# Optimization experiments

Measured on AMD Instinct MI355X. Metric: run time of the kernel, lower is better.

## Reference

```python
import jax, jax.numpy as jnp
import numpy as np

N = 100000      # nodes
E = 1200000     # edges
K = 512         # TopKPooling ratio=512 -> fixed k
EPS = 1e-7      # GENConv message eps
BN_EPS = 1e-5   # BatchNorm eps
NEG_SLOPE = 0.01  # LeakyReLU default


def _lin_init(key, fan_in, fan_out):
    k1, k2 = jax.random.split(key)
    s = 1.0 / np.sqrt(fan_in)
    w = jax.random.uniform(k1, (fan_in, fan_out), minval=-s, maxval=s, dtype=jnp.float32)
    b = jax.random.uniform(k2, (fan_out,), minval=-s, maxval=s, dtype=jnp.float32)
    return w, b


def setup_inputs() -> dict:
    key = jax.random.key(0)
    ks = jax.random.split(key, 12)
    pos = jax.random.normal(ks[0], (N, 3), dtype=jnp.float32)
    edge_index = jax.random.randint(ks[1], (2, E), 0, N, dtype=jnp.int64)
    # GENConv(3, 16): lin_src + MLP [16, 32, 16] (BatchNorm+ReLU on hidden)
    c1_lw, c1_lb = _lin_init(ks[2], 3, 16)
    c1_w1, c1_b1 = _lin_init(ks[3], 16, 32)
    c1_g1 = jnp.ones((32,), jnp.float32); c1_be1 = jnp.zeros((32,), jnp.float32)
    c1_w2, c1_b2 = _lin_init(ks[4], 32, 16)
    # GENConv(16, 64): lin_src + MLP [64, 128, 64]
    c2_lw, c2_lb = _lin_init(ks[5], 16, 64)
    c2_w1, c2_b1 = _lin_init(ks[6], 64, 128)
    c2_g1 = jnp.ones((128,), jnp.float32); c2_be1 = jnp.zeros((128,), jnp.float32)
    c2_w2, c2_b2 = _lin_init(ks[7], 128, 64)
    # TopKPooling score weight [in_channels]
    pool_w = jax.random.uniform(ks[8], (64,), minval=-1.0/8, maxval=1.0/8, dtype=jnp.float32)
    return dict(pos=pos, edge_index=edge_index,
                c1_lw=c1_lw, c1_lb=c1_lb, c1_w1=c1_w1, c1_b1=c1_b1,
                c1_g1=c1_g1, c1_be1=c1_be1, c1_w2=c1_w2, c1_b2=c1_b2,
                c2_lw=c2_lw, c2_lb=c2_lb, c2_w1=c2_w1, c2_b1=c2_b1,
                c2_g1=c2_g1, c2_be1=c2_be1, c2_w2=c2_w2, c2_b2=c2_b2,
                pool_w=pool_w)


def _genconv(x, src, dst, lw, lb, w1, b1, g1, be1, w2, b2):
    # lin_src (in_channels != out_channels)
    x = x @ lw + lb                                   # [N, C]
    # message: relu(x_j) + eps
    msg = jax.nn.relu(x[src]) + EPS                   # [E, C]
    # softmax aggregation (t = 1.0), per destination, per channel
    m = jax.ops.segment_max(msg, dst, num_segments=N) # [N, C]
    a = jnp.exp(msg - m[dst])
    denom = jax.ops.segment_sum(a, dst, num_segments=N)
    alpha = a / (denom[dst] + 1e-16)
    out = jax.ops.segment_sum(msg * alpha, dst, num_segments=N)
    out = out + x                                     # residual with dst features
    # MLP: Linear -> BatchNorm (train-mode stats) -> ReLU -> Linear
    h = out @ w1 + b1
    mu = h.mean(axis=0)
    var = h.var(axis=0)
    h = (h - mu) / jnp.sqrt(var + BN_EPS) * g1 + be1
    h = jax.nn.relu(h)
    return h @ w2 + b2


def reference(pos, edge_index,
              c1_lw, c1_lb, c1_w1, c1_b1, c1_g1, c1_be1, c1_w2, c1_b2,
              c2_lw, c2_lb, c2_w1, c2_b1, c2_g1, c2_be1, c2_w2, c2_b2,
              pool_w):
    src, dst = edge_index[0], edge_index[1]
    x = _genconv(pos, src, dst, c1_lw, c1_lb, c1_w1, c1_b1, c1_g1, c1_be1, c1_w2, c1_b2)
    x = jnp.where(x > 0, x, NEG_SLOPE * x)            # LeakyReLU
    x = _genconv(x, src, dst, c2_lw, c2_lb, c2_w1, c2_b1, c2_g1, c2_be1, c2_w2, c2_b2)
    x = jnp.where(x > 0, x, NEG_SLOPE * x)
    # TopKPooling: score = tanh(x . w / ||w||), select top K, gate selected features
    score = jnp.tanh((x @ pool_w) / jnp.linalg.norm(pool_w))  # [N]
    top_vals, perm = jax.lax.top_k(score, K)
    return x[perm] * top_vals[:, None]                # [K, 64]
```

## Files before the change

### kernel.cpp

```cpp
#include <hip/hip_runtime.h>
#include <stdint.h>

#define BLK 256

static constexpr float F_EPS = 1e-7f;
static constexpr float F_NEG = 0.01f;
static constexpr int   TOPK  = 512;
static constexpr int   NPART = 8;
static constexpr int   PBLK  = 128;

typedef unsigned long long u64;

__device__ __forceinline__ unsigned int ord_f32(float f) {
  unsigned int u = __float_as_uint(f);
  return (u & 0x80000000u) ? ~u : (u | 0x80000000u);
}

template<int CIN, int COUT, int TM, bool BN, bool LEAKY, bool STAT>
__global__ __launch_bounds__(256) void gemm_tile(const float* __restrict__ in,
    const float* __restrict__ W, const float* __restrict__ b,
    const float* __restrict__ scale, const float* __restrict__ shift,
    float* __restrict__ out, double* __restrict__ partial, int n) {
  constexpr int TN = COUT / 16;
  constexpr int NODES = 16 * TM;
  constexpr int KC = (CIN > 64) ? 64 : CIN;
  constexpr int NPAD = NODES + 4;
  __shared__ float xs[KC][NPAD];
  __shared__ float wsh[CIN * COUT];
  __shared__ float sB[COUT];
  __shared__ float sSc[BN ? CIN : 4];
  __shared__ float sSh[BN ? CIN : 4];
  for (int i = threadIdx.x; i < CIN * COUT; i += 256) wsh[i] = W[i];
  for (int i = threadIdx.x; i < COUT; i += 256) sB[i] = b[i];
  if constexpr (BN) {
    for (int i = threadIdx.x; i < CIN; i += 256) { sSc[i] = scale[i]; sSh[i] = shift[i]; }
  }
  __syncthreads();
  const int tn = threadIdx.x & 15;
  const int tj = threadIdx.x >> 4;
  const int node0 = blockIdx.x * NODES;

  float acc[TM][TN];
  #pragma unroll
  for (int m = 0; m < TM; ++m)
    #pragma unroll
    for (int j = 0; j < TN; ++j) acc[m][j] = sB[tj * TN + j];

  for (int kc = 0; kc < CIN; kc += KC) {
    __syncthreads();
    constexpr int NL = NODES * (KC / 4);
    for (int i = threadIdx.x; i < NL; i += 256) {
      int nd = i / (KC / 4);
      int kq = i - nd * (KC / 4);
      int gn = node0 + nd;
      const float* p = in + (size_t)(gn < n ? gn : n - 1) * CIN + kc + kq * 4;
      float4 v = *reinterpret_cast<const float4*>(p);
      if constexpr (BN) {
        int kb = kc + kq * 4;
        v.x = fmaxf(v.x * sSc[kb+0] + sSh[kb+0], 0.f);
        v.y = fmaxf(v.y * sSc[kb+1] + sSh[kb+1], 0.f);
        v.z = fmaxf(v.z * sSc[kb+2] + sSh[kb+2], 0.f);
        v.w = fmaxf(v.w * sSc[kb+3] + sSh[kb+3], 0.f);
      }
      xs[kq*4+0][nd] = v.x; xs[kq*4+1][nd] = v.y;
      xs[kq*4+2][nd] = v.z; xs[kq*4+3][nd] = v.w;
    }
    __syncthreads();
    #pragma unroll 16
    for (int k = 0; k < KC; ++k) {
      float xv[TM], wv[TN];
      #pragma unroll
      for (int m = 0; m < TM; ++m) xv[m] = xs[k][tn * TM + m];
      #pragma unroll
      for (int j = 0; j < TN; ++j) wv[j] = wsh[(kc + k) * COUT + tj * TN + j];
      #pragma unroll
      for (int m = 0; m < TM; ++m)
        #pragma unroll
        for (int j = 0; j < TN; ++j)
          acc[m][j] += xv[m] * wv[j];
    }
  }
  #pragma unroll
  for (int m = 0; m < TM; ++m) {
    int gn = node0 + tn * TM + m;
    if (gn < n) {
      float* orow = out + (size_t)gn * COUT + tj * TN;
      #pragma unroll
      for (int j = 0; j < TN; j += 4) {
        float a0 = acc[m][j], a1 = acc[m][j+1], a2 = acc[m][j+2], a3 = acc[m][j+3];
        if constexpr (LEAKY) {
          a0 = a0 > 0.f ? a0 : F_NEG * a0;
          a1 = a1 > 0.f ? a1 : F_NEG * a1;
          a2 = a2 > 0.f ? a2 : F_NEG * a2;
          a3 = a3 > 0.f ? a3 : F_NEG * a3;
        }
        float4 r; r.x = a0; r.y = a1; r.z = a2; r.w = a3;
        *reinterpret_cast<float4*>(orow + j) = r;
      }
    }
  }
  if constexpr (STAT) {
    __shared__ double sStat[2 * COUT];
    double sv[TN], qv[TN];
    #pragma unroll
    for (int j = 0; j < TN; ++j) { sv[j] = 0.0; qv[j] = 0.0; }
    #pragma unroll
    for (int m = 0; m < TM; ++m) {
      bool v = (node0 + tn * TM + m) < n;
      #pragma unroll
      for (int j = 0; j < TN; ++j) {
        double a = v ? (double)acc[m][j] : 0.0;
        sv[j] += a; qv[j] += a * a;
      }
    }
    #pragma unroll
    for (int j = 0; j < TN; ++j) {
      for (int off = 8; off; off >>= 1) {
        sv[j] += __shfl_down(sv[j], off, 16);
        qv[j] += __shfl_down(qv[j], off, 16);
      }
    }
    if (tn == 0) {
      #pragma unroll
      for (int j = 0; j < TN; ++j) {
        sStat[tj * TN + j] = sv[j];
        sStat[COUT + tj * TN + j] = qv[j];
      }
    }
    __syncthreads();
    for (int i = threadIdx.x; i < 2 * COUT; i += 256)
      partial[(size_t)blockIdx.x * (2 * COUT) + i] = sStat[i];
  }
}

template<int COUT>
__global__ __launch_bounds__(256) void bn_fin_ws(const double* __restrict__ partial,
    const float* __restrict__ g, const float* __restrict__ be,
    float* __restrict__ sc, float* __restrict__ sh, int n, int nbx) {
  int j = blockIdx.x;
  int t = threadIdx.x;
  double s = 0, q = 0;
  for (int bdx = t; bdx < nbx; bdx += 256) {
    s += partial[(size_t)bdx * (2 * COUT) + j];
    q += partial[(size_t)bdx * (2 * COUT) + COUT + j];
  }
  for (int off = 32; off; off >>= 1) { s += __shfl_down(s, off); q += __shfl_down(q, off); }
  __shared__ double sw[4][2];
  int lane = t & 63, wid = t >> 6;
  if (lane == 0) { sw[wid][0] = s; sw[wid][1] = q; }
  __syncthreads();
  if (t == 0) {
    s = sw[0][0] + sw[1][0] + sw[2][0] + sw[3][0];
    q = sw[0][1] + sw[1][1] + sw[2][1] + sw[3][1];
    double inv_n = 1.0 / (double)n;
    double mu = s * inv_n;
    double var = q * inv_n - mu * mu;
    double scd = (double)g[j] / sqrt(var + 1e-5);
    sc[j] = (float)scd;
    sh[j] = (float)((double)be[j] - mu * scd);
  }
}

template<int CIN, int COUT, int JT, bool STAT = false>
__global__ __launch_bounds__(BLK) void lin_kernel(const float* __restrict__ in,
    const float* __restrict__ W, const float* __restrict__ b,
    float* __restrict__ out, double* __restrict__ partial, int n) {
  __shared__ float sW[CIN * JT];
  __shared__ float sB[JT];
  const int j0 = blockIdx.y * JT;
  for (int i = threadIdx.x; i < CIN * JT; i += BLK) {
    int k = i / JT, jj = i - k * JT;
    sW[i] = W[k * COUT + j0 + jj];
  }
  for (int i = threadIdx.x; i < JT; i += BLK) sB[i] = b[j0 + i];
  __syncthreads();
  int node = blockIdx.x * BLK + threadIdx.x;
  bool valid = node < n;
  if constexpr (!STAT) { if (!valid) return; }
  int rnode = valid ? node : (n - 1);
  float acc[JT];
  #pragma unroll
  for (int jj = 0; jj < JT; ++jj) acc[jj] = sB[jj];
  const float* xrow = in + (size_t)rnode * CIN;
  if constexpr ((CIN & 3) == 0) {
    float x[CIN];
    #pragma unroll
    for (int k4 = 0; k4 < CIN / 4; ++k4) {
      float4 v = *reinterpret_cast<const float4*>(xrow + k4 * 4);
      x[4*k4+0] = v.x; x[4*k4+1] = v.y; x[4*k4+2] = v.z; x[4*k4+3] = v.w;
    }
    #pragma unroll
    for (int k = 0; k < CIN; ++k) {
      #pragma unroll
      for (int jj = 0; jj < JT; ++jj)
        acc[jj] += x[k] * sW[k * JT + jj];
    }
  } else {
    #pragma unroll
    for (int k = 0; k < CIN; ++k) {
      float xv = xrow[k];
      #pragma unroll
      for (int jj = 0; jj < JT; ++jj)
        acc[jj] += xv * sW[k * JT + jj];
    }
  }
  if (valid) {
    float* orow = out + (size_t)node * COUT + j0;
    #pragma unroll
    for (int jj = 0; jj < JT; jj += 4) {
      float4 r; r.x = acc[jj]; r.y = acc[jj+1]; r.z = acc[jj+2]; r.w = acc[jj+3];
      *reinterpret_cast<float4*>(orow + jj) = r;
    }
  }
  if constexpr (STAT) {
    __shared__ double sStat[4][2 * JT];
    int lane = threadIdx.x & 63, wid = threadIdx.x >> 6;
    #pragma unroll
    for (int jj = 0; jj < JT; ++jj) {
      double sv = valid ? (double)acc[jj] : 0.0;
      double qv = sv * sv;
      for (int off = 32; off; off >>= 1) {
        sv += __shfl_down(sv, off);
        qv += __shfl_down(qv, off);
      }
      if (lane == 0) { sStat[wid][jj] = sv; sStat[wid][JT + jj] = qv; }
    }
    __syncthreads();
    if (threadIdx.x < 2 * JT) {
      double v = sStat[0][threadIdx.x] + sStat[1][threadIdx.x]
               + sStat[2][threadIdx.x] + sStat[3][threadIdx.x];
      partial[((size_t)blockIdx.y * gridDim.x + blockIdx.x) * (2 * JT) + threadIdx.x] = v;
    }
  }
}

template<int COUT, int JT>
__global__ __launch_bounds__(256) void bn_fin3(const double* __restrict__ partial,
    const float* __restrict__ g, const float* __restrict__ be,
    float* __restrict__ sc, float* __restrict__ sh, int n, int nbx) {
  int j = blockIdx.x;
  int t = threadIdx.x;
  int jt = j / JT, jj = j - jt * JT;
  double s = 0, q = 0;
  for (int b = t; b < nbx; b += 256) {
    const double* row = partial + ((size_t)jt * nbx + b) * (2 * JT);
    s += row[jj];
    q += row[JT + jj];
  }
  for (int off = 32; off; off >>= 1) { s += __shfl_down(s, off); q += __shfl_down(q, off); }
  __shared__ double sw[4][2];
  int lane = t & 63, wid = t >> 6;
  if (lane == 0) { sw[wid][0] = s; sw[wid][1] = q; }
  __syncthreads();
  if (t == 0) {
    s = sw[0][0] + sw[1][0] + sw[2][0] + sw[3][0];
    q = sw[0][1] + sw[1][1] + sw[2][1] + sw[3][1];
    double inv_n = 1.0 / (double)n;
    double mu = s * inv_n;
    double var = q * inv_n - mu * mu;
    double scd = (double)g[j] / sqrt(var + 1e-5);
    sc[j] = (float)scd;
    sh[j] = (float)((double)be[j] - mu * scd);
  }
}

template<int CIN, int COUT, int JT>
__global__ __launch_bounds__(BLK) void mlp2_kernel(const float* __restrict__ h,
    const float* __restrict__ scale, const float* __restrict__ shift,
    const float* __restrict__ W, const float* __restrict__ b,
    float* __restrict__ out, int n) {
  __shared__ float sW[CIN * JT];
  __shared__ float sB[JT];
  __shared__ float sSc[CIN];
  __shared__ float sSh[CIN];
  const int j0 = blockIdx.y * JT;
  for (int i = threadIdx.x; i < CIN * JT; i += BLK) {
    int k = i / JT, jj = i - k * JT;
    sW[i] = W[k * COUT + j0 + jj];
  }
  for (int i = threadIdx.x; i < JT; i += BLK) sB[i] = b[j0 + i];
  for (int i = threadIdx.x; i < CIN; i += BLK) { sSc[i] = scale[i]; sSh[i] = shift[i]; }
  __syncthreads();
  int node = blockIdx.x * BLK + threadIdx.x;
  if (node >= n) return;
  float acc[JT];
  #pragma unroll
  for (int jj = 0; jj < JT; ++jj) acc[jj] = sB[jj];
  const float* xrow = h + (size_t)node * CIN;
  float x[CIN];
  #pragma unroll
  for (int k4 = 0; k4 < CIN / 4; ++k4) {
    float4 v = *reinterpret_cast<const float4*>(xrow + k4 * 4);
    x[4*k4+0] = fmaxf(v.x * sSc[4*k4+0] + sSh[4*k4+0], 0.f);
    x[4*k4+1] = fmaxf(v.y * sSc[4*k4+1] + sSh[4*k4+1], 0.f);
    x[4*k4+2] = fmaxf(v.z * sSc[4*k4+2] + sSh[4*k4+2], 0.f);
    x[4*k4+3] = fmaxf(v.w * sSc[4*k4+3] + sSh[4*k4+3], 0.f);
  }
  #pragma unroll
  for (int k = 0; k < CIN; ++k) {
    #pragma unroll
    for (int jj = 0; jj < JT; ++jj)
      acc[jj] += x[k] * sW[k * JT + jj];
  }
  float* orow = out + (size_t)node * COUT + j0;
  #pragma unroll
  for (int jj = 0; jj < JT; jj += 4) {
    float a0 = acc[jj], a1 = acc[jj+1], a2 = acc[jj+2], a3 = acc[jj+3];
    a0 = a0 > 0.f ? a0 : F_NEG * a0;
    a1 = a1 > 0.f ? a1 : F_NEG * a1;
    a2 = a2 > 0.f ? a2 : F_NEG * a2;
    a3 = a3 > 0.f ? a3 : F_NEG * a3;
    float4 r; r.x = a0; r.y = a1; r.z = a2; r.w = a3;
    *reinterpret_cast<float4*>(orow + jj) = r;
  }
}

__global__ __launch_bounds__(BLK) void deg_kernel(const int* __restrict__ dst,
    int* __restrict__ deg, int E) {
  int e = blockIdx.x * BLK + threadIdx.x;
  if (e < E) atomicAdd(&deg[dst[e]], 1);
}

__global__ __launch_bounds__(BLK) void blocksum_kernel(const int* __restrict__ deg,
    int* __restrict__ bsum, int n) {
  int i = blockIdx.x * BLK + threadIdx.x;
  int v = (i < n) ? deg[i] : 0;
  for (int off = 32; off; off >>= 1) v += __shfl_down(v, off);
  __shared__ int wsum[4];
  int lane = threadIdx.x & 63, wid = threadIdx.x >> 6;
  if (lane == 0) wsum[wid] = v;
  __syncthreads();
  if (threadIdx.x == 0) bsum[blockIdx.x] = wsum[0] + wsum[1] + wsum[2] + wsum[3];
}

__global__ __launch_bounds__(512) void scanb_kernel(int* __restrict__ bsum, int nb) {
  __shared__ int s[512];
  int t = threadIdx.x;
  int orig = (t < nb) ? bsum[t] : 0;
  s[t] = orig;
  __syncthreads();
  for (int off = 1; off < 512; off <<= 1) {
    int add = (t >= off) ? s[t - off] : 0;
    __syncthreads();
    s[t] += add;
    __syncthreads();
  }
  if (t < nb) bsum[t] = s[t] - orig;
}

__global__ __launch_bounds__(BLK) void rowstart_kernel(const int* __restrict__ deg,
    const int* __restrict__ bsum, int* __restrict__ rowstart,
    int* __restrict__ cursor, int n) {
  __shared__ int s[BLK];
  int t = threadIdx.x, i = blockIdx.x * BLK + t;
  int orig = (i < n) ? deg[i] : 0;
  s[t] = orig;
  __syncthreads();
  for (int off = 1; off < BLK; off <<= 1) {
    int add = (t >= off) ? s[t - off] : 0;
    __syncthreads();
    s[t] += add;
    __syncthreads();
  }
  if (i < n) { int st = bsum[blockIdx.x] + s[t] - orig; rowstart[i] = st; cursor[i] = st; }
}

__global__ __launch_bounds__(BLK) void scatter_kernel(const int* __restrict__ src,
    const int* __restrict__ dst, int* __restrict__ cursor, int* __restrict__ eidx,
    int E, int n) {
  const int r = blockIdx.x & (NPART - 1);
  const int sb = blockIdx.x >> 3;
  const int nsb = gridDim.x >> 3;
  for (int e = sb * BLK + threadIdx.x; e < E; e += nsb * BLK) {
    int d = dst[e];
    int dr = (int)(((unsigned long long)(unsigned)d * NPART) / (unsigned)n);
    if (dr == r) {
      int p = atomicAdd(&cursor[d], 1);
      eidx[p] = src[e];
    }
  }
}

template<int C>
__global__ __launch_bounds__(BLK) void agg_kernel(const int* __restrict__ rowstart,
    const int* __restrict__ deg, const int* __restrict__ eidx,
    const float* __restrict__ x, float* __restrict__ out, int n) {
  int gid = blockIdx.x * BLK + threadIdx.x;
  int node, c;
  if constexpr (C == 64) {
    node = __builtin_amdgcn_readfirstlane(gid >> 6);
    c = threadIdx.x & 63;
  } else {
    node = gid / C;
    c = gid & (C - 1);
  }
  if (node >= n) return;
  int s0, d;
  if constexpr (C == 64) {
    s0 = __builtin_amdgcn_readfirstlane(rowstart[node]);
    d  = __builtin_amdgcn_readfirstlane(deg[node]);
  } else {
    s0 = rowstart[node];
    d  = deg[node];
  }
  const float* xc = x + c;
  const int* ep = eidx + s0;
  float den = 0.f, num = 0.f;
  int nq = d >> 2;
  int i0 = 0, i1 = 0, i2 = 0, i3 = 0;
  int j0 = 0, j1 = 0, j2 = 0, j3 = 0;
  if (nq > 0) { i0 = ep[0]; i1 = ep[1]; i2 = ep[2]; i3 = ep[3]; }
  if (nq > 1) { j0 = ep[4]; j1 = ep[5]; j2 = ep[6]; j3 = ep[7]; }
  int q = 0;
  for (; q + 1 < nq; q += 2) {
    float xa = xc[(unsigned)i0 * C];
    float xb = xc[(unsigned)i1 * C];
    float xcv = xc[(unsigned)i2 * C];
    float xd = xc[(unsigned)i3 * C];
    float ya = xc[(unsigned)j0 * C];
    float yb = xc[(unsigned)j1 * C];
    float yc = xc[(unsigned)j2 * C];
    float yd = xc[(unsigned)j3 * C];
    if (q + 2 < nq) {
      const int* p2 = ep + (q + 2) * 4;
      i0 = p2[0]; i1 = p2[1]; i2 = p2[2]; i3 = p2[3];
    }
    if (q + 3 < nq) {
      const int* p3 = ep + (q + 3) * 4;
      j0 = p3[0]; j1 = p3[1]; j2 = p3[2]; j3 = p3[3];
    }
    float ma = fmaxf(xa, 0.f) + F_EPS;
    float mb = fmaxf(xb, 0.f) + F_EPS;
    float mc = fmaxf(xcv, 0.f) + F_EPS;
    float md = fmaxf(xd, 0.f) + F_EPS;
    float na = fmaxf(ya, 0.f) + F_EPS;
    float nb = fmaxf(yb, 0.f) + F_EPS;
    float nc = fmaxf(yc, 0.f) + F_EPS;
    float nd = fmaxf(yd, 0.f) + F_EPS;
    float aa = __expf(ma), ab = __expf(mb), ac = __expf(mc), ad = __expf(md);
    float ba = __expf(na), bb = __expf(nb), bc = __expf(nc), bd = __expf(nd);
    den += ((aa + ab) + (ac + ad)) + ((ba + bb) + (bc + bd));
    num += ((ma * aa + mb * ab) + (mc * ac + md * ad))
         + ((na * ba + nb * bb) + (nc * bc + nd * bd));
  }
  if (q < nq) {
    float xa = xc[(unsigned)i0 * C];
    float xb = xc[(unsigned)i1 * C];
    float xcv = xc[(unsigned)i2 * C];
    float xd = xc[(unsigned)i3 * C];
    float ma = fmaxf(xa, 0.f) + F_EPS;
    float mb = fmaxf(xb, 0.f) + F_EPS;
    float mc = fmaxf(xcv, 0.f) + F_EPS;
    float md = fmaxf(xd, 0.f) + F_EPS;
    float aa = __expf(ma), ab = __expf(mb), ac = __expf(mc), ad = __expf(md);
    den += (aa + ab) + (ac + ad);
    num += (ma * aa + mb * ab) + (mc * ac + md * ad);
  }
  for (int j = nq * 4; j < d; ++j) {
    int sA = ep[j];
    float xa = xc[(unsigned)sA * C];
    float ma = fmaxf(xa, 0.f) + F_EPS;
    float aa = __expf(ma);
    den += aa;
    num += ma * aa;
  }
  float xdv = xc[(unsigned)node * C];
  out[(size_t)node * C + c] = num / (den + 1e-16f) + xdv;
}

__global__ __launch_bounds__(BLK) void score_kernel(const float* __restrict__ x,
    const float* __restrict__ w, float* __restrict__ scores,
    u64* __restrict__ keys, int* __restrict__ ghist, int n) {
  __shared__ float sw[64];
  __shared__ float snorm;
  __shared__ int hl[256];
  if (threadIdx.x < 64) sw[threadIdx.x] = w[threadIdx.x];
  hl[threadIdx.x] = 0;
  __syncthreads();
  if (threadIdx.x < 64) {
    float v = sw[threadIdx.x];
    float sq = v * v;
    for (int off = 32; off; off >>= 1) sq += __shfl_down(sq, off);
    if (threadIdx.x == 0) snorm = 1.f / sqrtf(sq);
  }
  __syncthreads();
  int node = blockIdx.x * BLK + threadIdx.x;
  if (node < n) {
    const float4* row = reinterpret_cast<const float4*>(x + (size_t)node * 64);
    float acc = 0.f;
    #pragma unroll
    for (int k4 = 0; k4 < 16; ++k4) {
      float4 v = row[k4];
      const float4 wv = *reinterpret_cast<const float4*>(&sw[4 * k4]);
      acc += v.x * wv.x + v.y * wv.y + v.z * wv.z + v.w * wv.w;
    }
    float s = tanhf(acc * snorm);
    scores[node] = s;
    u64 key = ((u64)ord_f32(s) << 17) | (u64)(0x1FFFF - node);
    keys[node] = key;
    atomicAdd(&hl[(int)(key >> 41)], 1);
  }
  __syncthreads();
  int v = hl[threadIdx.x];
  if (v) atomicAdd(&ghist[threadIdx.x], v);
}

__global__ void pick0_kernel(int* __restrict__ istate, const int* __restrict__ hist) {
  if (threadIdx.x == 0) {
    int k = TOPK, run = 0;
    for (int d = 255; d >= 0; --d) {
      int c = hist[d];
      if (run + c >= k) { istate[1] = d; istate[0] = k - run; break; }
      run += c;
    }
    istate[2] = 0; istate[4] = 0;
  }
}

__global__ __launch_bounds__(BLK) void compact0_kernel(const u64* __restrict__ in,
    u64* __restrict__ outb, u64* __restrict__ sel, int* __restrict__ istate, int n) {
  int i = blockIdx.x * BLK + threadIdx.x;
  if (i >= n) return;
  u64 kkey = in[i];
  int b = (int)(kkey >> 41);
  int digit = istate[1];
  if (b > digit) {
    sel[atomicAdd(&istate[2], 1)] = kkey;
  } else if (b == digit) {
    outb[atomicAdd(&istate[4], 1)] = kkey;
  }
}

__global__ __launch_bounds__(1024) void topk_finish(u64* __restrict__ bufB,
    u64* __restrict__ bufA, u64* __restrict__ sel, const int* __restrict__ istate,
    const float* __restrict__ scores, int* __restrict__ perm,
    float* __restrict__ gval) {
  __shared__ int hl[512];
  __shared__ int tsum[512];
  __shared__ u64 sk[512];
  __shared__ int sh_digit, sh_k, sh_sel, sh_out, sh_cnt;
  int t = threadIdx.x;
  if (t == 0) { sh_cnt = istate[4]; sh_k = istate[0]; sh_sel = istate[2]; }
  __syncthreads();
  u64* cur = bufB;
  u64* nxt = bufA;
  const int shifts[5] = {33, 25, 17, 9, 0};
  const int masks[5]  = {255, 255, 255, 255, 511};
  for (int r = 0; r < 5; ++r) {
    const int shift = shifts[r], mask = masks[r], wlen = mask + 1;
    for (int i = t; i < wlen; i += 1024) hl[i] = 0;
    __syncthreads();
    int cnt = sh_cnt, krem = sh_k;
    for (int i = t; i < cnt; i += 1024)
      atomicAdd(&hl[(int)(cur[i] >> shift) & mask], 1);
    __syncthreads();
    int v = 0;
    if (t < wlen) { v = hl[t]; tsum[t] = v; }
    __syncthreads();
    for (int off = 1; off < wlen; off <<= 1) {
      int add = 0;
      if (t + off < wlen) add = tsum[t + off];
      __syncthreads();
      if (t + off < wlen) tsum[t] += add;
      __syncthreads();
    }
    if (t < wlen) {
      int T = tsum[t];
      if (T >= krem && (T - v) < krem) {
        sh_digit = t;
        sh_k = krem - (T - v);
      }
    }
    if (t == 0) sh_out = 0;
    __syncthreads();
    int digit = sh_digit;
    for (int i = t; i < cnt; i += 1024) {
      u64 kk = cur[i];
      int b = (int)(kk >> shift) & mask;
      if (b > digit) sel[atomicAdd(&sh_sel, 1)] = kk;
      else if (b == digit) nxt[atomicAdd(&sh_out, 1)] = kk;
    }
    __syncthreads();
    if (t == 0) sh_cnt = sh_out;
    __syncthreads();
    u64* tmp = cur; cur = nxt; nxt = tmp;
  }
  int base = sh_sel, krem = sh_k;
  for (int i = t; i < krem; i += 1024) sel[base + i] = cur[i];
  __syncthreads();
  if (t < 512) sk[t] = sel[t];
  __syncthreads();
  if (t < 512) {
    u64 key = sk[t];
    int rank = 0;
    for (int j = 0; j < 512; ++j) rank += (sk[j] > key) ? 1 : 0;
    int node = 0x1FFFF - (int)(key & 0x1FFFFull);
    perm[rank] = node;
    gval[rank] = scores[node];
  }
}

__global__ __launch_bounds__(256) void gather_kernel(const int* __restrict__ perm,
    const float* __restrict__ gval, const float* __restrict__ x,
    float* __restrict__ out) {
  int i = blockIdx.x * 256 + threadIdx.x;
  int r = i >> 4, c = i & 15;
  int node = perm[r];
  float v = gval[r];
  float4 xv = reinterpret_cast<const float4*>(x)[(size_t)node * 16 + c];
  float4 o; o.x = xv.x * v; o.y = xv.y * v; o.z = xv.z * v; o.w = xv.w * v;
  reinterpret_cast<float4*>(out)[(size_t)r * 16 + c] = o;
}

extern "C" void kernel_launch(void* const* d_in, const int* in_sizes, int n_in,
                              void* d_out, int out_size, void* d_ws, size_t ws_size,
                              hipStream_t stream) {
  const int N = in_sizes[0] / 3;
  const int E = in_sizes[1] / 2;

  const float* pos   = (const float*)d_in[0];
  const int*   ei    = (const int*)d_in[1];
  const int*   src   = ei;
  const int*   dst   = ei + E;
  const float* c1_lw = (const float*)d_in[2];
  const float* c1_lb = (const float*)d_in[3];
  const float* c1_w1 = (const float*)d_in[4];
  const float* c1_b1 = (const float*)d_in[5];
  const float* c1_g1 = (const float*)d_in[6];
  const float* c1_be1= (const float*)d_in[7];
  const float* c1_w2 = (const float*)d_in[8];
  const float* c1_b2 = (const float*)d_in[9];
  const float* c2_lw = (const float*)d_in[10];
  const float* c2_lb = (const float*)d_in[11];
  const float* c2_w1 = (const float*)d_in[12];
  const float* c2_b1 = (const float*)d_in[13];
  const float* c2_g1 = (const float*)d_in[14];
  const float* c2_be1= (const float*)d_in[15];
  const float* c2_w2 = (const float*)d_in[16];
  const float* c2_b2 = (const float*)d_in[17];
  const float* poolw = (const float*)d_in[18];

  float* ws = (float*)d_ws;
  float* x1   = ws;
  float* h1   = ws + (size_t)16 * N;
  float* o1   = ws + (size_t)48 * N;
  float* res2 = ws;
  float* x2   = ws + (size_t)64 * N;
  float* res1 = x2;
  float* h2   = ws + (size_t)128 * N;
  float* o2   = ws + (size_t)256 * N;
  float* scores = ws + (size_t)320 * N;
  u64* candA = (u64*)(ws + (size_t)321 * N);
  u64* candB = candA + N;
  u64* sel   = candB + N;
  double* partial = (double*)(sel + TOPK);
  int* ibase   = (int*)(partial + (size_t)524288);
  int* istate  = ibase;
  int* hist    = ibase + 8;
  int* bsum    = ibase + 264;
  int* perm    = ibase + 776;
  float* gval  = (float*)(ibase + 1288);
  int* deg     = ibase + 1800;
  int* rowstart= deg + N;
  int* cursor  = rowstart + N;
  int* eidx    = cursor + N;
  float* fsc   = (float*)(eidx + E);
  float* sc1 = fsc;        float* sh1 = fsc + 32;
  float* sc2 = fsc + 64;   float* sh2 = fsc + 192;

  const int nbN = (N + BLK - 1) / BLK;
  const int nbE = (E + BLK - 1) / BLK;
  const int nbG = (N + 63) / 64;

  hipMemsetAsync(ibase, 0, (size_t)(1800 + N) * sizeof(int), stream);

  deg_kernel<<<nbE, BLK, 0, stream>>>(dst, deg, E);
  blocksum_kernel<<<nbN, BLK, 0, stream>>>(deg, bsum, N);
  scanb_kernel<<<1, 512, 0, stream>>>(bsum, nbN);
  rowstart_kernel<<<nbN, BLK, 0, stream>>>(deg, bsum, rowstart, cursor, N);
  scatter_kernel<<<NPART * PBLK, BLK, 0, stream>>>(src, dst, cursor, eidx, E, N);

  lin_kernel<3, 16, 16><<<dim3(nbN, 1), BLK, 0, stream>>>(pos, c1_lw, c1_lb, x1, nullptr, N);
  agg_kernel<16><<<(N * 16 + BLK - 1) / BLK, BLK, 0, stream>>>(rowstart, deg, eidx, x1, res1, N);
  lin_kernel<16, 32, 32, true><<<dim3(nbN, 1), BLK, 0, stream>>>(res1, c1_w1, c1_b1, h1, partial, N);
  bn_fin3<32, 32><<<32, 256, 0, stream>>>(partial, c1_g1, c1_be1, sc1, sh1, N, nbN);
  mlp2_kernel<32, 16, 16><<<dim3(nbN, 1), BLK, 0, stream>>>(h1, sc1, sh1, c1_w2, c1_b2, o1, N);

  gemm_tile<16, 64, 4, false, false, false><<<nbG, 256, 0, stream>>>(
      o1, c2_lw, c2_lb, nullptr, nullptr, x2, nullptr, N);
  agg_kernel<64><<<(N * 64 + BLK - 1) / BLK, BLK, 0, stream>>>(rowstart, deg, eidx, x2, res2, N);
  gemm_tile<64, 128, 4, false, false, true><<<nbG, 256, 0, stream>>>(
      res2, c2_w1, c2_b1, nullptr, nullptr, h2, partial, N);
  bn_fin_ws<128><<<128, 256, 0, stream>>>(partial, c2_g1, c2_be1, sc2, sh2, N, nbG);
  gemm_tile<128, 64, 4, true, true, false><<<nbG, 256, 0, stream>>>(
      h2, c2_w2, c2_b2, sc2, sh2, o2, nullptr, N);

  score_kernel<<<nbN, BLK, 0, stream>>>(o2, poolw, scores, candA, hist, N);
  pick0_kernel<<<1, 64, 0, stream>>>(istate, hist);
  compact0_kernel<<<nbN, BLK, 0, stream>>>(candA, candB, sel, istate, N);
  topk_finish<<<1, 1024, 0, stream>>>(candB, candA, sel, istate, scores, perm, gval);
  gather_kernel<<<32, 256, 0, stream>>>(perm, gval, o2, (float*)d_out);

  (void)n_in; (void)out_size; (void)ws_size;
}
```

Before: 381.0 us.

## Pre-bucket edges by destination partition before CSR scatter

```diff
diff --git a/kernel.cpp b/kernel.cpp
--- a/kernel.cpp
+++ b/kernel.cpp
@@ -8,6 +8,7 @@
 static constexpr int   TOPK  = 512;
 static constexpr int   NPART = 8;
 static constexpr int   PBLK  = 128;
+static constexpr int   PBN   = 1024;
 
 typedef unsigned long long u64;
 
@@ -365,19 +366,76 @@
   if (i < n) { int st = bsum[blockIdx.x] + s[t] - orig; rowstart[i] = st; cursor[i] = st; }
 }
 
-__global__ __launch_bounds__(BLK) void scatter_kernel(const int* __restrict__ src,
-    const int* __restrict__ dst, int* __restrict__ cursor, int* __restrict__ eidx,
-    int E, int n) {
+__global__ __launch_bounds__(BLK) void pcount_kernel(const int* __restrict__ dst,
+    int* __restrict__ pcnt, int E, int step, int chunk) {
+  __shared__ int c8[NPART];
+  if (threadIdx.x < NPART) c8[threadIdx.x] = 0;
+  __syncthreads();
+  int e0 = blockIdx.x * chunk;
+  int e1 = min(e0 + chunk, E);
+  for (int e = e0 + threadIdx.x; e < e1; e += BLK) {
+    int p = dst[e] / step;
+    if (p > NPART - 1) p = NPART - 1;
+    atomicAdd(&c8[p], 1);
+  }
+  __syncthreads();
+  if (threadIdx.x < NPART) pcnt[blockIdx.x * NPART + threadIdx.x] = c8[threadIdx.x];
+}
+
+__global__ __launch_bounds__(1024) void pscan_kernel(const int* __restrict__ pcnt,
+    int* __restrict__ poff, int* __restrict__ ptot, int nb) {
+  __shared__ int s[1024];
+  __shared__ int colbase;
+  int t = threadIdx.x;
+  if (t == 0) colbase = 0;
+  __syncthreads();
+  for (int p = 0; p < NPART; ++p) {
+    int orig = (t < nb) ? pcnt[t * NPART + p] : 0;
+    s[t] = orig;
+    __syncthreads();
+    for (int off = 1; off < 1024; off <<= 1) {
+      int add = (t >= off) ? s[t - off] : 0;
+      __syncthreads();
+      s[t] += add;
+      __syncthreads();
+    }
+    if (t < nb) poff[t * NPART + p] = colbase + s[t] - orig;
+    if (t == 0) ptot[p] = colbase;
+    __syncthreads();
+    if (t == 0) colbase += s[1023];
+    __syncthreads();
+  }
+  if (t == 0) ptot[NPART] = colbase;
+}
+
+__global__ __launch_bounds__(BLK) void ppack_kernel(const int* __restrict__ src,
+    const int* __restrict__ dst, const int* __restrict__ poff,
+    int2* __restrict__ pairbuf, int E, int step, int chunk) {
+  __shared__ int c8[NPART];
+  if (threadIdx.x < NPART) c8[threadIdx.x] = poff[blockIdx.x * NPART + threadIdx.x];
+  __syncthreads();
+  int e0 = blockIdx.x * chunk;
+  int e1 = min(e0 + chunk, E);
+  for (int e = e0 + threadIdx.x; e < e1; e += BLK) {
+    int d = dst[e], s = src[e];
+    int p = d / step;
+    if (p > NPART - 1) p = NPART - 1;
+    int pos = atomicAdd(&c8[p], 1);
+    pairbuf[pos] = make_int2(s, d);
+  }
+}
+
+__global__ __launch_bounds__(BLK) void scatter2_kernel(const int2* __restrict__ pairbuf,
+    const int* __restrict__ ptot, int* __restrict__ cursor, int* __restrict__ eidx) {
   const int r = blockIdx.x & (NPART - 1);
+  const int s0 = ptot[r];
+  const int s1 = ptot[r + 1];
   const int sb = blockIdx.x >> 3;
   const int nsb = gridDim.x >> 3;
-  for (int e = sb * BLK + threadIdx.x; e < E; e += nsb * BLK) {
-    int d = dst[e];
-    int dr = (int)(((unsigned long long)(unsigned)d * NPART) / (unsigned)n);
-    if (dr == r) {
-      int p = atomicAdd(&cursor[d], 1);
-      eidx[p] = src[e];
-    }
+  for (int i = s0 + sb * BLK + threadIdx.x; i < s1; i += nsb * BLK) {
+    int2 pr = pairbuf[i];
+    int p = atomicAdd(&cursor[pr.y], 1);
+    eidx[p] = pr.x;
   }
 }
 
@@ -667,10 +725,16 @@
   float* fsc   = (float*)(eidx + E);
   float* sc1 = fsc;        float* sh1 = fsc + 32;
   float* sc2 = fsc + 64;   float* sh2 = fsc + 192;
+  int2* pairbuf = (int2*)(((uintptr_t)(fsc + 320) + 7) & ~(uintptr_t)7);
+  int* pcnt = (int*)(pairbuf + E);
+  int* poff = pcnt + PBN * NPART;
+  int* ptot = poff + PBN * NPART;
 
   const int nbN = (N + BLK - 1) / BLK;
   const int nbE = (E + BLK - 1) / BLK;
   const int nbG = (N + 63) / 64;
+  const int step = N / NPART;
+  const int chunk = (E + PBN - 1) / PBN;
 
   hipMemsetAsync(ibase, 0, (size_t)(1800 + N) * sizeof(int), stream);
 
@@ -678,7 +742,10 @@
   blocksum_kernel<<<nbN, BLK, 0, stream>>>(deg, bsum, N);
   scanb_kernel<<<1, 512, 0, stream>>>(bsum, nbN);
   rowstart_kernel<<<nbN, BLK, 0, stream>>>(deg, bsum, rowstart, cursor, N);
-  scatter_kernel<<<NPART * PBLK, BLK, 0, stream>>>(src, dst, cursor, eidx, E, N);
+  pcount_kernel<<<PBN, BLK, 0, stream>>>(dst, pcnt, E, step, chunk);
+  pscan_kernel<<<1, 1024, 0, stream>>>(pcnt, poff, ptot, PBN);
+  ppack_kernel<<<PBN, BLK, 0, stream>>>(src, dst, poff, pairbuf, E, step, chunk);
+  scatter2_kernel<<<NPART * PBLK, BLK, 0, stream>>>(pairbuf, ptot, cursor, eidx);
 
   lin_kernel<3, 16, 16><<<dim3(nbN, 1), BLK, 0, stream>>>(pos, c1_lw, c1_lb, x1, nullptr, N);
   agg_kernel<16><<<(N * 16 + BLK - 1) / BLK, BLK, 0, stream>>>(rowstart, deg, eidx, x1, res1, N);
```

After: 407.7 us. 7.0% more time.

## Build CSR via two-level bucket sort instead of global atomic scatter

Applied to the files above, without the earlier changes.

```diff
diff --git a/kernel.cpp b/kernel.cpp
--- a/kernel.cpp
+++ b/kernel.cpp
@@ -6,8 +6,10 @@
 static constexpr float F_EPS = 1e-7f;
 static constexpr float F_NEG = 0.01f;
 static constexpr int   TOPK  = 512;
-static constexpr int   NPART = 8;
-static constexpr int   PBLK  = 128;
+static constexpr int   PA    = 128;
+static constexpr int   BSH   = 9;
+static constexpr int   MAXBUK= 256;
+static constexpr int   CAP   = 8192;
 
 typedef unsigned long long u64;
 
@@ -349,8 +351,7 @@
 }
 
 __global__ __launch_bounds__(BLK) void rowstart_kernel(const int* __restrict__ deg,
-    const int* __restrict__ bsum, int* __restrict__ rowstart,
-    int* __restrict__ cursor, int n) {
+    const int* __restrict__ bsum, int* __restrict__ rowstart, int n) {
   __shared__ int s[BLK];
   int t = threadIdx.x, i = blockIdx.x * BLK + t;
   int orig = (i < n) ? deg[i] : 0;
@@ -362,21 +363,97 @@
     s[t] += add;
     __syncthreads();
   }
-  if (i < n) { int st = bsum[blockIdx.x] + s[t] - orig; rowstart[i] = st; cursor[i] = st; }
-}
-
-__global__ __launch_bounds__(BLK) void scatter_kernel(const int* __restrict__ src,
-    const int* __restrict__ dst, int* __restrict__ cursor, int* __restrict__ eidx,
-    int E, int n) {
-  const int r = blockIdx.x & (NPART - 1);
-  const int sb = blockIdx.x >> 3;
-  const int nsb = gridDim.x >> 3;
-  for (int e = sb * BLK + threadIdx.x; e < E; e += nsb * BLK) {
-    int d = dst[e];
-    int dr = (int)(((unsigned long long)(unsigned)d * NPART) / (unsigned)n);
-    if (dr == r) {
-      int p = atomicAdd(&cursor[d], 1);
-      eidx[p] = src[e];
+  if (i < n) rowstart[i] = bsum[blockIdx.x] + s[t] - orig;
+}
+
+__global__ __launch_bounds__(BLK) void pcount_kernel(const int* __restrict__ dst,
+    int* __restrict__ pcnt, int E, int chunk) {
+  __shared__ int cb[MAXBUK];
+  for (int i = threadIdx.x; i < MAXBUK; i += BLK) cb[i] = 0;
+  __syncthreads();
+  int e0 = blockIdx.x * chunk;
+  int e1 = min(e0 + chunk, E);
+  for (int e = e0 + threadIdx.x; e < e1; e += BLK)
+    atomicAdd(&cb[dst[e] >> BSH], 1);
+  __syncthreads();
+  for (int i = threadIdx.x; i < MAXBUK; i += BLK)
+    pcnt[blockIdx.x * MAXBUK + i] = cb[i];
+}
+
+__global__ __launch_bounds__(256) void pscan_kernel(const int* __restrict__ pcnt,
+    int* __restrict__ poff, int* __restrict__ ptot, int nblk, int nbuk) {
+  __shared__ int s[256];
+  __shared__ int tot[256];
+  int t = threadIdx.x;
+  int sum = 0;
+  if (t < nbuk) {
+    for (int blk = 0; blk < nblk; ++blk) {
+      int v = pcnt[blk * MAXBUK + t];
+      poff[blk * MAXBUK + t] = sum;
+      sum += v;
+    }
+  }
+  tot[t] = (t < nbuk) ? sum : 0;
+  s[t] = tot[t];
+  __syncthreads();
+  for (int off = 1; off < 256; off <<= 1) {
+    int add = (t >= off) ? s[t - off] : 0;
+    __syncthreads();
+    s[t] += add;
+    __syncthreads();
+  }
+  if (t < nbuk) ptot[t] = s[t] - tot[t];
+  if (t == 0) ptot[nbuk] = s[255];
+}
+
+__global__ __launch_bounds__(BLK) void ppack_kernel(const int* __restrict__ src,
+    const int* __restrict__ dst, const int* __restrict__ poff,
+    const int* __restrict__ ptot, int* __restrict__ pairbuf, int E, int chunk) {
+  __shared__ int cb[MAXBUK];
+  for (int i = threadIdx.x; i < MAXBUK; i += BLK)
+    cb[i] = ptot[i] + poff[blockIdx.x * MAXBUK + i];
+  __syncthreads();
+  int e0 = blockIdx.x * chunk;
+  int e1 = min(e0 + chunk, E);
+  for (int e = e0 + threadIdx.x; e < e1; e += BLK) {
+    int d = dst[e], sv = src[e];
+    int b = d >> BSH;
+    int pos = atomicAdd(&cb[b], 1);
+    pairbuf[pos] = ((d & ((1 << BSH) - 1)) << 17) | sv;
+  }
+}
+
+__global__ __launch_bounds__(BLK) void place_kernel(const int* __restrict__ pairbuf,
+    const int* __restrict__ ptot, const int* __restrict__ rowstart,
+    int* __restrict__ eidx, int n, int E) {
+  __shared__ int lcur[1 << BSH];
+  __shared__ int seg[CAP];
+  const int b = blockIdx.x;
+  const int n0 = b << BSH;
+  const int nn = min(1 << BSH, n - n0);
+  const int base = rowstart[n0];
+  const int segend = (n0 + (1 << BSH) >= n) ? E : rowstart[n0 + (1 << BSH)];
+  const int seglen = segend - base;
+  for (int i = threadIdx.x; i < nn; i += BLK)
+    lcur[i] = rowstart[n0 + i] - base;
+  __syncthreads();
+  const int p0 = ptot[b], p1 = ptot[b + 1];
+  if (seglen <= CAP) {
+    for (int i = p0 + threadIdx.x; i < p1; i += BLK) {
+      int pk = pairbuf[i];
+      int dloc = pk >> 17;
+      int pos = atomicAdd(&lcur[dloc], 1);
+      seg[pos] = pk & 0x1FFFF;
+    }
+    __syncthreads();
+    for (int i = threadIdx.x; i < seglen; i += BLK)
+      eidx[base + i] = seg[i];
+  } else {
+    for (int i = p0 + threadIdx.x; i < p1; i += BLK) {
+      int pk = pairbuf[i];
+      int dloc = pk >> 17;
+      int pos = atomicAdd(&lcur[dloc], 1);
+      eidx[base + pos] = pk & 0x1FFFF;
     }
   }
 }
@@ -662,23 +739,31 @@
   float* gval  = (float*)(ibase + 1288);
   int* deg     = ibase + 1800;
   int* rowstart= deg + N;
-  int* cursor  = rowstart + N;
-  int* eidx    = cursor + N;
-  float* fsc   = (float*)(eidx + E);
+  int* eidx    = rowstart + N;
+  int* pairbuf = eidx + E;
+  int* pcnt    = pairbuf + E;
+  int* poff    = pcnt + PA * MAXBUK;
+  int* ptot    = poff + PA * MAXBUK;
+  float* fsc   = (float*)(ptot + MAXBUK + 1);
   float* sc1 = fsc;        float* sh1 = fsc + 32;
   float* sc2 = fsc + 64;   float* sh2 = fsc + 192;
 
   const int nbN = (N + BLK - 1) / BLK;
   const int nbE = (E + BLK - 1) / BLK;
   const int nbG = (N + 63) / 64;
+  const int NBUK = (N + (1 << BSH) - 1) >> BSH;
+  const int chunk = (E + PA - 1) / PA;
 
   hipMemsetAsync(ibase, 0, (size_t)(1800 + N) * sizeof(int), stream);
 
   deg_kernel<<<nbE, BLK, 0, stream>>>(dst, deg, E);
   blocksum_kernel<<<nbN, BLK, 0, stream>>>(deg, bsum, N);
   scanb_kernel<<<1, 512, 0, stream>>>(bsum, nbN);
-  rowstart_kernel<<<nbN, BLK, 0, stream>>>(deg, bsum, rowstart, cursor, N);
-  scatter_kernel<<<NPART * PBLK, BLK, 0, stream>>>(src, dst, cursor, eidx, E, N);
+  rowstart_kernel<<<nbN, BLK, 0, stream>>>(deg, bsum, rowstart, N);
+  pcount_kernel<<<PA, BLK, 0, stream>>>(dst, pcnt, E, chunk);
+  pscan_kernel<<<1, 256, 0, stream>>>(pcnt, poff, ptot, PA, NBUK);
+  ppack_kernel<<<PA, BLK, 0, stream>>>(src, dst, poff, ptot, pairbuf, E, chunk);
+  place_kernel<<<NBUK, BLK, 0, stream>>>(pairbuf, ptot, rowstart, eidx, N, E);
 
   lin_kernel<3, 16, 16><<<dim3(nbN, 1), BLK, 0, stream>>>(pos, c1_lw, c1_lb, x1, nullptr, N);
   agg_kernel<16><<<(N * 16 + BLK - 1) / BLK, BLK, 0, stream>>>(rowstart, deg, eidx, x1, res1, N);
```

After: 395.5 us. 3.8% more time.
